# Optimization experiments

Hardware: AMD Instinct MI355X
Metric: run time of the kernel (lower is better)

## Reference

```python
import jax, jax.numpy as jnp
import numpy as np
from jax import lax

# ---- ConvBlock config (matches init_kwargs) ----
IN_CH, OUT_CH, K, MB = 64, 128, 3, 8
P = OUT_CH // MB            # 16 block-rows
Q = (IN_CH * K * K) // MB   # 72 block-cols (64*9=576, divisible by 8)
BN_EPS = 1e-5
ACT_THRES = 6.0


def setup_inputs() -> dict:
    key = jax.random.key(0)
    k1, k2, k3, k4 = jax.random.split(key, 4)
    x = jax.random.normal(k1, (32, IN_CH, 56, 56), dtype=jnp.float32)
    # block-decomposed MZI weight: [p, q, mb, mb]
    fan_in = IN_CH * K * K
    w_blocks = jax.random.normal(k2, (P, Q, MB, MB), dtype=jnp.float32) * (1.0 / np.sqrt(fan_in))
    gamma = jax.random.uniform(k3, (OUT_CH,), dtype=jnp.float32, minval=0.5, maxval=1.5)
    beta = jax.random.normal(k4, (OUT_CH,), dtype=jnp.float32) * 0.1
    return {"x": x, "w_blocks": w_blocks, "gamma": gamma, "beta": beta}


def _assemble_weight(w_blocks):
    # [p, q, mb, mb] -> dense [p*mb, q*mb] -> crop -> [O, I, K, K]
    p, q, mb, _ = w_blocks.shape
    w = jnp.transpose(w_blocks, (0, 2, 1, 3)).reshape(p * mb, q * mb)
    w = w[:OUT_CH, : IN_CH * K * K]
    return w.reshape(OUT_CH, IN_CH, K, K)


def reference(x, w_blocks, gamma, beta):
    # MZIBlockConv2d, weight mode, w_bit=in_bit=16 => quantizers are identity,
    # photodetect=False => plain real-valued conv with block-assembled weight.
    w = _assemble_weight(w_blocks)
    y = lax.conv_general_dilated(
        x, w,
        window_strides=(1, 1),
        padding=((1, 1), (1, 1)),
        dimension_numbers=("NCHW", "OIHW", "NCHW"),
    )
    # BatchNorm2d in training mode: batch statistics over (N, H, W), biased var
    mean = jnp.mean(y, axis=(0, 2, 3))
    var = jnp.var(y, axis=(0, 2, 3))
    inv = gamma / jnp.sqrt(var + BN_EPS)
    y = (y - mean[None, :, None, None]) * inv[None, :, None, None] + beta[None, :, None, None]
    # ReLUN(6): clipped ReLU
    return jnp.clip(y, 0.0, ACT_THRES)
```

## Files before the change

kernel.cpp:

```cpp
#include <hip/hip_runtime.h>

#define NB    32
#define CIN   64
#define COUT  128
#define HH    56
#define WW    56
#define NPIX  (NB*HH*WW)
#define BN_EPSF 1e-5f

typedef __bf16 bf16x8 __attribute__((ext_vector_type(8)));
typedef float  f32x4  __attribute__((ext_vector_type(4)));

__global__ void zero_sums(float* g) {
    g[threadIdx.x] = 0.0f;
}

__global__ void assemble_w(const float* __restrict__ wb, __bf16* __restrict__ whi) {
    int idx = blockIdx.x * 256 + threadIdx.x;
    if (idx >= 576 * 128) return;
    int col = idx >> 7, oc = idx & 127;
    int p = oc >> 3, i = oc & 7, q = col >> 3, j = col & 7;
    float v = wb[((p * 72 + q) * 8 + i) * 8 + j];
    int ic = col / 9, tap = col % 9;
    int dst = ((tap * 2 + (ic >> 5)) * 128 + oc) * 32 + (ic & 31);
    whi[dst] = (__bf16)v;
}

__global__ __launch_bounds__(256, 8) void conv_mfma(
    const float* __restrict__ x, const __bf16* __restrict__ whi,
    float* __restrict__ y, float* __restrict__ gsum, float* __restrict__ gsq)
{
    __shared__ __bf16 xs[100 * 64];

    int b = blockIdx.x;
    int n = b / 49, t = b % 49;
    int h0 = (t / 7) * 8, w0 = (t % 7) * 8;
    int tid  = threadIdx.x;
    int lane = tid & 63, wid = tid >> 6;
    int l15 = lane & 15, l4 = lane >> 4;
    int oc0 = wid * 32;

    const float* xn = x + n * CIN * HH * WW;
    for (int u = tid; u < 800; u += 256) {
        int c = u / 100, px = u - c * 100;
        int r = px / 10, cc = px - r * 10;
        int gh = h0 - 1 + r, gw = w0 - 1 + cc;
        bool ok = ((unsigned)gh < 56u) & ((unsigned)gw < 56u);
        const float* src = xn + (c * 8) * (HH * WW) + gh * WW + gw;
        bf16x8 hv;
        #pragma unroll
        for (int j = 0; j < 8; ++j) {
            float v = ok ? src[j * HH * WW] : 0.0f;
            hv[j] = (__bf16)v;
        }
        *(bf16x8*)&xs[px * 64 + ((c ^ (px & 7)) * 8)] = hv;
    }
    __syncthreads();

    f32x4 acc[4][2] = {};

    int rb0  = (l15 >> 3) * 10 + (l15 & 7);
    int woff = (oc0 + l15) * 32 + l4 * 8;

    #pragma unroll 2
    for (int th = 0; th < 18; ++th) {
        int tap = th >> 1, half = th & 1;
        int kh = (tap * 11) >> 5;
        int toff = kh * 10 + (tap - kh * 3);
        const __bf16* bp = whi + th * 4096;
        bf16x8 b0 = *(const bf16x8*)&bp[woff];
        bf16x8 b1 = *(const bf16x8*)&bp[woff + 512];
        int c0 = half * 4 + l4;
        #pragma unroll
        for (int mt = 0; mt < 4; ++mt) {
            int R  = rb0 + mt * 20 + toff;
            int ae = R * 64 + ((c0 ^ (R & 7)) * 8);
            bf16x8 ah = *(const bf16x8*)&xs[ae];
            acc[mt][0] = __builtin_amdgcn_mfma_f32_16x16x32_bf16(ah, b0, acc[mt][0], 0, 0, 0);
            acc[mt][1] = __builtin_amdgcn_mfma_f32_16x16x32_bf16(ah, b1, acc[mt][1], 0, 0, 0);
        }
    }

    float* yn = y + n * COUT * HH * WW;
    int pyb = l4 >> 1;
    int gwo = w0 + (l4 & 1) * 4;
    #pragma unroll
    for (int mt = 0; mt < 4; ++mt) {
        int gh = h0 + mt * 2 + pyb;
        #pragma unroll
        for (int nt = 0; nt < 2; ++nt) {
            int oc = oc0 + nt * 16 + l15;
            *(float4*)&yn[(oc * HH + gh) * WW + gwo] = *(float4*)&acc[mt][nt];
        }
    }

    float* red = (float*)xs;
    __syncthreads();
    #pragma unroll
    for (int nt = 0; nt < 2; ++nt) {
        float s = 0.0f, sq = 0.0f;
        #pragma unroll
        for (int mt = 0; mt < 4; ++mt)
            #pragma unroll
            for (int r = 0; r < 4; ++r) {
                float v = acc[mt][nt][r];
                s += v; sq += v * v;
            }
        s  += __shfl_xor(s, 16, 64);  s  += __shfl_xor(s, 32, 64);
        sq += __shfl_xor(sq, 16, 64); sq += __shfl_xor(sq, 32, 64);
        if (l4 == 0) {
            int oc = oc0 + nt * 16 + l15;
            red[oc] = s; red[128 + oc] = sq;
        }
    }
    __syncthreads();
    if (tid < 128) {
        atomicAdd(&gsum[tid], red[tid]);
        atomicAdd(&gsq[tid],  red[128 + tid]);
    }
}

__global__ void bn_finalize(const float* __restrict__ gsum, const float* __restrict__ gsq,
                            const float* __restrict__ gamma, const float* __restrict__ beta,
                            float* __restrict__ scale, float* __restrict__ shift)
{
    int c = threadIdx.x;
    float mean = gsum[c] * (1.0f / NPIX);
    float var  = gsq[c]  * (1.0f / NPIX) - mean * mean;
    float inv  = gamma[c] / sqrtf(var + BN_EPSF);
    scale[c] = inv;
    shift[c] = beta[c] - mean * inv;
}

__global__ __launch_bounds__(256) void bn_apply(float* __restrict__ y,
        const float* __restrict__ scale, const float* __restrict__ shift)
{
    const int total4 = NB * COUT * HH * WW / 4;
    int idx = blockIdx.x * blockDim.x + threadIdx.x;
    int stride = gridDim.x * blockDim.x;
    for (int i4 = idx; i4 < total4; i4 += stride) {
        int c = (i4 / 784) & 127;
        float sc = scale[c], sh = shift[c];
        float4 v = ((float4*)y)[i4];
        v.x = fminf(fmaxf(fmaf(v.x, sc, sh), 0.0f), 6.0f);
        v.y = fminf(fmaxf(fmaf(v.y, sc, sh), 0.0f), 6.0f);
        v.z = fminf(fmaxf(fmaf(v.z, sc, sh), 0.0f), 6.0f);
        v.w = fminf(fmaxf(fmaf(v.w, sc, sh), 0.0f), 6.0f);
        ((float4*)y)[i4] = v;
    }
}

extern "C" void kernel_launch(void* const* d_in, const int* in_sizes, int n_in,
                              void* d_out, int out_size, void* d_ws, size_t ws_size,
                              hipStream_t stream) {
    const float* x     = (const float*)d_in[0];
    const float* wb    = (const float*)d_in[1];
    const float* gamma = (const float*)d_in[2];
    const float* beta  = (const float*)d_in[3];
    float* y = (float*)d_out;

    __bf16* whi = (__bf16*)d_ws;
    float* gsum  = (float*)(whi + 73728);
    float* gsq   = gsum + 128;
    float* scale = gsq + 128;
    float* shift = scale + 128;

    zero_sums<<<1, 256, 0, stream>>>(gsum);
    assemble_w<<<(576 * 128 + 255) / 256, 256, 0, stream>>>(wb, whi);
    conv_mfma<<<NB * 49, 256, 0, stream>>>(x, whi, y, gsum, gsq);
    bn_finalize<<<1, COUT, 0, stream>>>(gsum, gsq, gamma, beta, scale, shift);
    bn_apply<<<2048, 256, 0, stream>>>(y, scale, shift);
}
```

Baseline: 173.7 us.

## Pre-pad input to bf16 and split conv blocks across output-channel halves

Measured after the change: 185.5 us. 1.07x slower.

```diff
diff --git a/kernel.cpp b/kernel.cpp
--- a/kernel.cpp
+++ b/kernel.cpp
@@ -5,118 +5,127 @@
 #define COUT  128
 #define HH    56
 #define WW    56
+#define HP    58
 #define NPIX  (NB*HH*WW)
 #define BN_EPSF 1e-5f
+
+#define NXPAD (NB*CIN*HP*HP)
 
 typedef __bf16 bf16x8 __attribute__((ext_vector_type(8)));
 typedef float  f32x4  __attribute__((ext_vector_type(4)));
 
-__global__ void zero_sums(float* g) {
-    g[threadIdx.x] = 0.0f;
+__global__ __launch_bounds__(256) void prep(
+    const float* __restrict__ x, const float* __restrict__ wb,
+    __bf16* __restrict__ xpad, __bf16* __restrict__ whi, float* __restrict__ gsum)
+{
+    int idx = blockIdx.x * 256 + threadIdx.x;
+    if (idx < NXPAD) {
+        int wp = idx % HP, r = idx / HP;
+        int hp = r % HP, ci = r / HP;
+        __bf16 v = (__bf16)0.0f;
+        if (hp >= 1 && hp <= 56 && wp >= 1 && wp <= 56)
+            v = (__bf16)x[(ci * HH + (hp - 1)) * WW + (wp - 1)];
+        xpad[idx] = v;
+        return;
+    }
+    idx -= NXPAD;
+    if (idx < 576 * 128) {
+        int col = idx >> 7, oc = idx & 127;
+        int p = oc >> 3, i = oc & 7, q = col >> 3, j = col & 7;
+        float v = wb[((p * 72 + q) * 8 + i) * 8 + j];
+        int ic = col / 9, tap = col % 9;
+        int dst = ((tap * 2 + (ic >> 5)) * 128 + oc) * 32 + (ic & 31);
+        whi[dst] = (__bf16)v;
+        return;
+    }
+    idx -= 576 * 128;
+    if (idx < 256) gsum[idx] = 0.0f;
 }
 
-__global__ void assemble_w(const float* __restrict__ wb, __bf16* __restrict__ whi) {
-    int idx = blockIdx.x * 256 + threadIdx.x;
-    if (idx >= 576 * 128) return;
-    int col = idx >> 7, oc = idx & 127;
-    int p = oc >> 3, i = oc & 7, q = col >> 3, j = col & 7;
-    float v = wb[((p * 72 + q) * 8 + i) * 8 + j];
-    int ic = col / 9, tap = col % 9;
-    int dst = ((tap * 2 + (ic >> 5)) * 128 + oc) * 32 + (ic & 31);
-    whi[dst] = (__bf16)v;
-}
-
-__global__ __launch_bounds__(256, 8) void conv_mfma(
-    const float* __restrict__ x, const __bf16* __restrict__ whi,
+__global__ __launch_bounds__(256, 4) void conv_mfma(
+    const __bf16* __restrict__ xpad, const __bf16* __restrict__ whi,
     float* __restrict__ y, float* __restrict__ gsum, float* __restrict__ gsq)
 {
     __shared__ __bf16 xs[100 * 64];
 
     int b = blockIdx.x;
-    int n = b / 49, t = b % 49;
+    int ocb = b & 1;
+    int tile = b >> 1;
+    int n = tile / 49, t = tile % 49;
     int h0 = (t / 7) * 8, w0 = (t % 7) * 8;
     int tid  = threadIdx.x;
     int lane = tid & 63, wid = tid >> 6;
     int l15 = lane & 15, l4 = lane >> 4;
-    int oc0 = wid * 32;
+    int oc0 = ocb * 64 + wid * 16;
 
-    const float* xn = x + n * CIN * HH * WW;
+    int woff = (oc0 + l15) * 32 + l4 * 8;
+    bf16x8 barr[18];
+    #pragma unroll
+    for (int th = 0; th < 18; ++th)
+        barr[th] = *(const bf16x8*)&whi[th * 4096 + woff];
+
+    const __bf16* xn = xpad + n * CIN * HP * HP;
     for (int u = tid; u < 800; u += 256) {
         int c = u / 100, px = u - c * 100;
         int r = px / 10, cc = px - r * 10;
-        int gh = h0 - 1 + r, gw = w0 - 1 + cc;
-        bool ok = ((unsigned)gh < 56u) & ((unsigned)gw < 56u);
-        const float* src = xn + (c * 8) * (HH * WW) + gh * WW + gw;
+        const __bf16* src = xn + (c * 8) * (HP * HP) + (h0 + r) * HP + (w0 + cc);
         bf16x8 hv;
         #pragma unroll
-        for (int j = 0; j < 8; ++j) {
-            float v = ok ? src[j * HH * WW] : 0.0f;
-            hv[j] = (__bf16)v;
-        }
+        for (int j = 0; j < 8; ++j) hv[j] = src[j * HP * HP];
         *(bf16x8*)&xs[px * 64 + ((c ^ (px & 7)) * 8)] = hv;
     }
     __syncthreads();
 
-    f32x4 acc[4][2] = {};
+    f32x4 acc[4] = {};
+    int rb0 = (l15 >> 3) * 10 + (l15 & 7);
 
-    int rb0  = (l15 >> 3) * 10 + (l15 & 7);
-    int woff = (oc0 + l15) * 32 + l4 * 8;
-
-    #pragma unroll 2
+    #pragma unroll
     for (int th = 0; th < 18; ++th) {
-        int tap = th >> 1, half = th & 1;
-        int kh = (tap * 11) >> 5;
-        int toff = kh * 10 + (tap - kh * 3);
-        const __bf16* bp = whi + th * 4096;
-        bf16x8 b0 = *(const bf16x8*)&bp[woff];
-        bf16x8 b1 = *(const bf16x8*)&bp[woff + 512];
+        const int tap = th >> 1, half = th & 1;
+        const int kh = tap / 3, kw = tap - kh * 3;
+        const int toff = kh * 10 + kw;
         int c0 = half * 4 + l4;
         #pragma unroll
         for (int mt = 0; mt < 4; ++mt) {
             int R  = rb0 + mt * 20 + toff;
             int ae = R * 64 + ((c0 ^ (R & 7)) * 8);
             bf16x8 ah = *(const bf16x8*)&xs[ae];
-            acc[mt][0] = __builtin_amdgcn_mfma_f32_16x16x32_bf16(ah, b0, acc[mt][0], 0, 0, 0);
-            acc[mt][1] = __builtin_amdgcn_mfma_f32_16x16x32_bf16(ah, b1, acc[mt][1], 0, 0, 0);
+            acc[mt] = __builtin_amdgcn_mfma_f32_16x16x32_bf16(ah, barr[th], acc[mt], 0, 0, 0);
         }
     }
 
     float* yn = y + n * COUT * HH * WW;
     int pyb = l4 >> 1;
     int gwo = w0 + (l4 & 1) * 4;
+    int oc  = oc0 + l15;
     #pragma unroll
     for (int mt = 0; mt < 4; ++mt) {
         int gh = h0 + mt * 2 + pyb;
-        #pragma unroll
-        for (int nt = 0; nt < 2; ++nt) {
-            int oc = oc0 + nt * 16 + l15;
-            *(float4*)&yn[(oc * HH + gh) * WW + gwo] = *(float4*)&acc[mt][nt];
-        }
+        *(float4*)&yn[(oc * HH + gh) * WW + gwo] = *(float4*)&acc[mt];
     }
 
     float* red = (float*)xs;
     __syncthreads();
-    #pragma unroll
-    for (int nt = 0; nt < 2; ++nt) {
+    {
         float s = 0.0f, sq = 0.0f;
         #pragma unroll
         for (int mt = 0; mt < 4; ++mt)
             #pragma unroll
             for (int r = 0; r < 4; ++r) {
-                float v = acc[mt][nt][r];
+                float v = acc[mt][r];
                 s += v; sq += v * v;
             }
         s  += __shfl_xor(s, 16, 64);  s  += __shfl_xor(s, 32, 64);
         sq += __shfl_xor(sq, 16, 64); sq += __shfl_xor(sq, 32, 64);
         if (l4 == 0) {
-            int oc = oc0 + nt * 16 + l15;
-            red[oc] = s; red[128 + oc] = sq;
+            int o = wid * 16 + l15;
+            red[o] = s; red[64 + o] = sq;
         }
     }
     __syncthreads();
-    if (tid < 128) {
-        atomicAdd(&gsum[tid], red[tid]);
-        atomicAdd(&gsq[tid],  red[128 + tid]);
+    if (tid < 64) {
+        atomicAdd(&gsum[ocb * 64 + tid], red[tid]);
+        atomicAdd(&gsq [ocb * 64 + tid], red[64 + tid]);
     }
 }
 
@@ -159,15 +168,16 @@
     const float* beta  = (const float*)d_in[3];
     float* y = (float*)d_out;
 
-    __bf16* whi = (__bf16*)d_ws;
+    __bf16* xpad = (__bf16*)d_ws;
+    __bf16* whi  = xpad + NXPAD;
     float* gsum  = (float*)(whi + 73728);
     float* gsq   = gsum + 128;
     float* scale = gsq + 128;
     float* shift = scale + 128;
 
-    zero_sums<<<1, 256, 0, stream>>>(gsum);
-    assemble_w<<<(576 * 128 + 255) / 256, 256, 0, stream>>>(wb, whi);
-    conv_mfma<<<NB * 49, 256, 0, stream>>>(x, whi, y, gsum, gsq);
+    int prep_grid = (NXPAD + 576 * 128 + 256 + 255) / 256;
+    prep<<<prep_grid, 256, 0, stream>>>(x, wb, xpad, whi, gsum);
+    conv_mfma<<<NB * 49 * 2, 256, 0, stream>>>(xpad, whi, y, gsum, gsq);
     bn_finalize<<<1, COUT, 0, stream>>>(gsum, gsq, gamma, beta, scale, shift);
     bn_apply<<<2048, 256, 0, stream>>>(y, scale, shift);
 }
```
